# Optimization experiments

Measured on AMD Instinct MI355X. Metric: run time of the kernel, lower is better.

## Reference

```python
import jax, jax.numpy as jnp
import numpy as np

H_RENDER = 640   # hard-coded render resolution in the torch forward
W_RENDER = 640
OUT_H = 128      # self.height
OUT_W = 128      # self.width
NUM_VERTS = 778  # MANO hand mesh
NUM_FACES = 1538
BATCH = 4
BG_DEPTH = 1e10  # z-buffer background, clamped to 100 afterwards


def setup_inputs() -> dict:
    key = jax.random.key(0)
    k1, k2, k3 = jax.random.split(key, 3)
    # screen-space x,y in [0, 640), positive depth z
    xy = jax.random.uniform(k1, (BATCH, NUM_VERTS, 2), minval=0.0, maxval=640.0)
    z = jax.random.uniform(k2, (BATCH, NUM_VERTS, 1), minval=0.3, maxval=1.5)
    vertices = jnp.concatenate([xy, z], axis=-1).astype(jnp.float32)
    faces = jax.random.randint(k3, (NUM_FACES, 3), 0, NUM_VERTS)
    # right_hand=True: swap face columns 0 and 1 (winding flip), as in __init__
    faces = faces[:, jnp.array([1, 0, 2])].astype(jnp.int64)
    return {"vertices": vertices, "faces": faces}


def _edge(ax, ay, bx, by, px, py):
    # signed area of (a, b, p); standard rasterizer edge function
    return (bx - ax) * (py - ay) - (by - ay) * (px - ax)


def _rasterize(face_vertices):
    # face_vertices: [B, F, 3(vertex), 3(x,y,z)] -> z-buffer depth map [B, H, W]
    B = face_vertices.shape[0]
    ys, xs = jnp.meshgrid(
        jnp.arange(H_RENDER, dtype=jnp.float32) + 0.5,
        jnp.arange(W_RENDER, dtype=jnp.float32) + 0.5,
        indexing='ij',
    )  # pixel centers, [H, W]

    def step(zbuf, tri):
        # tri: [B, 3, 3] -> per-vertex coords broadcast to [B, 1, 1]
        x = tri[:, :, 0][:, :, None, None]
        y = tri[:, :, 1][:, :, None, None]
        z = tri[:, :, 2][:, :, None, None]
        x0, x1, x2 = x[:, 0], x[:, 1], x[:, 2]
        y0, y1, y2 = y[:, 0], y[:, 1], y[:, 2]
        z0, z1, z2 = z[:, 0], z[:, 1], z[:, 2]
        e0 = _edge(x1, y1, x2, y2, xs, ys)  # weight of v0
        e1 = _edge(x2, y2, x0, y0, xs, ys)  # weight of v1
        e2 = _edge(x0, y0, x1, y1, xs, ys)  # weight of v2
        area = _edge(x0, y0, x1, y1, x2, y2)  # [B,1,1]
        s = jnp.sign(area)
        valid = jnp.abs(area) > 1e-12
        inside = (e0 * s >= 0) & (e1 * s >= 0) & (e2 * s >= 0) & valid
        safe_area = jnp.where(valid, area, 1.0)
        zpix = (e0 * z0 + e1 * z1 + e2 * z2) / safe_area  # barycentric depth
        cand = jnp.where(inside, zpix, jnp.float32(BG_DEPTH))
        return jnp.minimum(zbuf, cand), None

    zbuf0 = jnp.full((B, H_RENDER, W_RENDER), BG_DEPTH, dtype=jnp.float32)
    zbuf, _ = jax.lax.scan(step, zbuf0, jnp.swapaxes(face_vertices, 0, 1))
    return zbuf


def reference(vertices, faces):
    B = vertices.shape[0]
    F = faces.shape[0]
    # vertex gather: vertices[:, faces.view(-1), 0:3].view(B, F, 3, 3)
    fv = vertices[:, faces.reshape(-1), 0:3].reshape(B, F, 3, 3)
    dm = _rasterize(fv)
    dm = jnp.minimum(dm, 100.0)  # torch.clamp(max=100.0)
    # bilinear resize, align_corners=False (half-pixel), no antialias, like F.interpolate
    resized = jax.image.resize(dm[:, None], (B, 1, OUT_H, OUT_W), method='linear', antialias=False)
    return resized[:, 0]
```

## Files before the change

kernel.cpp:

```cpp
#include <hip/hip_runtime.h>


#pragma clang fp contract(off)

#define H_OUT 128
#define W_OUT 128
#define NV 778
#define NF 1538
#define NB 4
#define NCHUNK 25
#define NFP (NCHUNK * 64)
#define BG100 0x42C80000u


__global__ __launch_bounds__(256) void prep_kernel(
    const float* __restrict__ verts,
    const int* __restrict__ faces,
    float* __restrict__ bbox,
    float* __restrict__ data,
    unsigned int* __restrict__ outu)
{
    int t = blockIdx.x * 256 + threadIdx.x;
    outu[t] = BG100;
    if (t >= NB * NFP) return;
    int b = t / NFP;
    int f = t - b * NFP;
    float* bb = bbox + (size_t)t * 4;
    if (f >= NF) {
        bb[0] = 1e30f; bb[1] = -1e30f; bb[2] = 1e30f; bb[3] = -1e30f;
        return;
    }
    int i0 = faces[f * 3 + 0];
    int i1 = faces[f * 3 + 1];
    int i2 = faces[f * 3 + 2];
    const float* vb = verts + (size_t)b * NV * 3;
    float x0 = vb[i0 * 3 + 0], y0 = vb[i0 * 3 + 1], z0 = vb[i0 * 3 + 2];
    float x1 = vb[i1 * 3 + 0], y1 = vb[i1 * 3 + 1], z1 = vb[i1 * 3 + 2];
    float x2 = vb[i2 * 3 + 0], y2 = vb[i2 * 3 + 1], z2 = vb[i2 * 3 + 2];

    float dx12 = x2 - x1, dy12 = y2 - y1;
    float dx02 = x0 - x2, dy02 = y0 - y2;
    float dx01 = x1 - x0, dy01 = y1 - y0;
    float y20 = y2 - y0, x20 = x2 - x0;
    float area = dx01 * y20 - dy01 * x20;

    float s = 0.0f;
    if (fabsf(area) > 1e-12f) s = (area > 0.0f) ? 1.0f : -1.0f;

    float xmin = fminf(fminf(x0, x1), x2), xmax = fmaxf(fmaxf(x0, x1), x2);
    float ymin = fminf(fminf(y0, y1), y2), ymax = fmaxf(fmaxf(y0, y1), y2);
    if (s == 0.0f) { xmin = 1e30f; xmax = -1e30f; }

    bb[0] = xmin; bb[1] = xmax; bb[2] = ymin; bb[3] = ymax;

    float* o = data + (size_t)t * 16;
    o[0] = s * dx12; o[1] = s * dy12;
    o[2] = s * dx02; o[3] = s * dy02;
    o[4] = s * dx01; o[5] = s * dy01;
    o[6] = x0;  o[7] = y0;  o[8] = x1;  o[9] = y1;  o[10] = x2; o[11] = y2;
    o[12] = z0; o[13] = z1; o[14] = z2; o[15] = s * area;
}

__global__ __launch_bounds__(128) void raster_kernel(
    const float* __restrict__ bbox,
    const float* __restrict__ data,
    unsigned int* __restrict__ outu)
{
    int blk = blockIdx.x;
    int tile  = blk & 127;
    int b     = (blk >> 7) & 3;
    int chunk = blk >> 9;
    int tid = threadIdx.x;
    int lane = tid & 63;
    int w = __builtin_amdgcn_readfirstlane(tid >> 6);

    int tx = tile & 7, ty = tile >> 3;
    int i = ty * 8 + w * 4 + (lane >> 4);
    int j = tx * 16 + (lane & 15);
    float px = 5.0f * (float)j + 2.5f;
    float py = 5.0f * (float)i + 2.5f;

    float px_lo = 80.0f * (float)tx + 2.5f, px_hi = px_lo + 75.0f;
    float py_lo = 40.0f * (float)ty + 20.0f * (float)w + 2.5f;
    float py_hi = py_lo + 15.0f;

    int gbase = b * NFP + chunk * 64;
    float4 bb = *(const float4*)&bbox[(size_t)(gbase + lane) * 4];
    bool ov = !(bb.x > px_hi || bb.y < px_lo || bb.z > py_hi || bb.w < py_lo);
    unsigned long long mask = __ballot(ov);

    float nb = 1e10f, ab = 1.0f;
    while (mask) {
        int f0 = __builtin_ctzll(mask); mask &= mask - 1;
        int f1 = mask ? __builtin_ctzll(mask) : f0;
        mask &= mask - 1;

        int u0 = __builtin_amdgcn_readfirstlane(f0);
        int u1 = __builtin_amdgcn_readfirstlane(f1);
        const float4* p0 = (const float4*)(data + (size_t)(gbase + u0) * 16);
        const float4* p1 = (const float4*)(data + (size_t)(gbase + u1) * 16);
        float4 A0 = p0[0], B0 = p0[1], C0 = p0[2], D0 = p0[3];
        float4 A1 = p1[0], B1 = p1[1], C1 = p1[2], D1 = p1[3];

        float e0 = A0.x * (py - C0.y) - A0.y * (px - C0.x);
        float e1 = A0.z * (py - C0.w) - A0.w * (px - C0.z);
        float e2 = B0.x * (py - B0.w) - B0.y * (px - B0.z);
        bool in0 = (e0 >= 0.0f) & (e1 >= 0.0f) & (e2 >= 0.0f);
        float n0 = ((e0 * D0.x) + (e1 * D0.y)) + (e2 * D0.z);
        bool t0 = in0 & (n0 * ab < nb * D0.w);
        nb = t0 ? n0 : nb;  ab = t0 ? D0.w : ab;

        float g0 = A1.x * (py - C1.y) - A1.y * (px - C1.x);
        float g1 = A1.z * (py - C1.w) - A1.w * (px - C1.z);
        float g2 = B1.x * (py - B1.w) - B1.y * (px - B1.z);
        bool in1 = (g0 >= 0.0f) & (g1 >= 0.0f) & (g2 >= 0.0f);
        float n1 = ((g0 * D1.x) + (g1 * D1.y)) + (g2 * D1.z);
        bool t1 = in1 & (n1 * ab < nb * D1.w);
        nb = t1 ? n1 : nb;  ab = t1 ? D1.w : ab;
    }

    float z = nb / ab;
    z += 0.0f;
    if (z < 1e9f)
        atomicMin(&outu[(size_t)b * (H_OUT * W_OUT) + i * W_OUT + j],
                  __float_as_uint(fminf(z, 100.0f)));
}

extern "C" void kernel_launch(void* const* d_in, const int* in_sizes, int n_in,
                              void* d_out, int out_size, void* d_ws, size_t ws_size,
                              hipStream_t stream) {
    const float* verts = (const float*)d_in[0];
    const int*   faces = (const int*)d_in[1];
    float* out = (float*)d_out;
    float* bbox = (float*)d_ws;
    float* data = bbox + (size_t)NB * NFP * 4;

    prep_kernel<<<256, 256, 0, stream>>>(verts, faces, bbox, data,
                                         (unsigned int*)out);
    raster_kernel<<<NCHUNK * NB * 128, 128, 0, stream>>>(
        bbox, data, (unsigned int*)out);
}
```

Before: 93.00 us.

## Process four pixel rows per lane with one wave per 16x16 tile

```diff
diff --git a/kernel.cpp b/kernel.cpp
--- a/kernel.cpp
+++ b/kernel.cpp
@@ -61,35 +61,38 @@
     o[12] = z0; o[13] = z1; o[14] = z2; o[15] = s * area;
 }
 
-__global__ __launch_bounds__(128) void raster_kernel(
+__global__ __launch_bounds__(64) void raster_kernel(
     const float* __restrict__ bbox,
     const float* __restrict__ data,
     unsigned int* __restrict__ outu)
 {
     int blk = blockIdx.x;
-    int tile  = blk & 127;
-    int b     = (blk >> 7) & 3;
-    int chunk = blk >> 9;
-    int tid = threadIdx.x;
-    int lane = tid & 63;
-    int w = __builtin_amdgcn_readfirstlane(tid >> 6);
+    int tile  = blk & 63;
+    int b     = (blk >> 6) & 3;
+    int chunk = blk >> 8;
+    int lane = threadIdx.x;
 
     int tx = tile & 7, ty = tile >> 3;
-    int i = ty * 8 + w * 4 + (lane >> 4);
-    int j = tx * 16 + (lane & 15);
-    float px = 5.0f * (float)j + 2.5f;
-    float py = 5.0f * (float)i + 2.5f;
+    int col = lane & 15;
+    int rg  = lane >> 4;
+    int j = tx * 16 + col;
+    int i0r = ty * 16 + rg;
+    float px  = 5.0f * (float)j + 2.5f;
+    float py0 = 5.0f * (float)i0r + 2.5f;
 
     float px_lo = 80.0f * (float)tx + 2.5f, px_hi = px_lo + 75.0f;
-    float py_lo = 40.0f * (float)ty + 20.0f * (float)w + 2.5f;
-    float py_hi = py_lo + 15.0f;
+    float py_lo = 80.0f * (float)ty + 2.5f, py_hi = py_lo + 75.0f;
 
     int gbase = b * NFP + chunk * 64;
     float4 bb = *(const float4*)&bbox[(size_t)(gbase + lane) * 4];
     bool ov = !(bb.x > px_hi || bb.y < px_lo || bb.z > py_hi || bb.w < py_lo);
     unsigned long long mask = __ballot(ov);
 
-    float nb = 1e10f, ab = 1.0f;
+    float nb0 = 1e10f, ab0 = 1.0f;
+    float nb1 = 1e10f, ab1 = 1.0f;
+    float nb2 = 1e10f, ab2 = 1.0f;
+    float nb3 = 1e10f, ab3 = 1.0f;
+
     while (mask) {
         int f0 = __builtin_ctzll(mask); mask &= mask - 1;
         int f1 = mask ? __builtin_ctzll(mask) : f0;
@@ -102,28 +105,43 @@
         float4 A0 = p0[0], B0 = p0[1], C0 = p0[2], D0 = p0[3];
         float4 A1 = p1[0], B1 = p1[1], C1 = p1[2], D1 = p1[3];
 
-        float e0 = A0.x * (py - C0.y) - A0.y * (px - C0.x);
-        float e1 = A0.z * (py - C0.w) - A0.w * (px - C0.z);
-        float e2 = B0.x * (py - B0.w) - B0.y * (px - B0.z);
-        bool in0 = (e0 >= 0.0f) & (e1 >= 0.0f) & (e2 >= 0.0f);
-        float n0 = ((e0 * D0.x) + (e1 * D0.y)) + (e2 * D0.z);
-        bool t0 = in0 & (n0 * ab < nb * D0.w);
-        nb = t0 ? n0 : nb;  ab = t0 ? D0.w : ab;
+        #pragma unroll
+        for (int k = 0; k < 4; ++k) {
+            float py = py0 + 20.0f * (float)k;
+            float* nbp = (k == 0) ? &nb0 : (k == 1) ? &nb1 : (k == 2) ? &nb2 : &nb3;
+            float* abp = (k == 0) ? &ab0 : (k == 1) ? &ab1 : (k == 2) ? &ab2 : &ab3;
+            float nb = *nbp, ab = *abp;
 
-        float g0 = A1.x * (py - C1.y) - A1.y * (px - C1.x);
-        float g1 = A1.z * (py - C1.w) - A1.w * (px - C1.z);
-        float g2 = B1.x * (py - B1.w) - B1.y * (px - B1.z);
-        bool in1 = (g0 >= 0.0f) & (g1 >= 0.0f) & (g2 >= 0.0f);
-        float n1 = ((g0 * D1.x) + (g1 * D1.y)) + (g2 * D1.z);
-        bool t1 = in1 & (n1 * ab < nb * D1.w);
-        nb = t1 ? n1 : nb;  ab = t1 ? D1.w : ab;
+            float e0 = A0.x * (py - C0.y) - A0.y * (px - C0.x);
+            float e1 = A0.z * (py - C0.w) - A0.w * (px - C0.z);
+            float e2 = B0.x * (py - B0.w) - B0.y * (px - B0.z);
+            bool in0 = (e0 >= 0.0f) & (e1 >= 0.0f) & (e2 >= 0.0f);
+            float n0 = ((e0 * D0.x) + (e1 * D0.y)) + (e2 * D0.z);
+            bool t0 = in0 & (n0 * ab < nb * D0.w);
+            nb = t0 ? n0 : nb;  ab = t0 ? D0.w : ab;
+
+            float h0 = A1.x * (py - C1.y) - A1.y * (px - C1.x);
+            float h1 = A1.z * (py - C1.w) - A1.w * (px - C1.z);
+            float h2 = B1.x * (py - B1.w) - B1.y * (px - B1.z);
+            bool in1 = (h0 >= 0.0f) & (h1 >= 0.0f) & (h2 >= 0.0f);
+            float n1 = ((h0 * D1.x) + (h1 * D1.y)) + (h2 * D1.z);
+            bool t1 = in1 & (n1 * ab < nb * D1.w);
+            nb = t1 ? n1 : nb;  ab = t1 ? D1.w : ab;
+
+            *nbp = nb; *abp = ab;
+        }
     }
 
-    float z = nb / ab;
-    z += 0.0f;
-    if (z < 1e9f)
-        atomicMin(&outu[(size_t)b * (H_OUT * W_OUT) + i * W_OUT + j],
-                  __float_as_uint(fminf(z, 100.0f)));
+    unsigned int* slot0 = &outu[(size_t)b * (H_OUT * W_OUT) + i0r * W_OUT + j];
+    #pragma unroll
+    for (int k = 0; k < 4; ++k) {
+        float nb = (k == 0) ? nb0 : (k == 1) ? nb1 : (k == 2) ? nb2 : nb3;
+        float ab = (k == 0) ? ab0 : (k == 1) ? ab1 : (k == 2) ? ab2 : ab3;
+        float z = nb / ab;
+        z += 0.0f;
+        if (z < 1e9f)
+            atomicMin(slot0 + k * 4 * W_OUT, __float_as_uint(fminf(z, 100.0f)));
+    }
 }
 
 extern "C" void kernel_launch(void* const* d_in, const int* in_sizes, int n_in,
@@ -137,6 +155,6 @@
 
     prep_kernel<<<256, 256, 0, stream>>>(verts, faces, bbox, data,
                                          (unsigned int*)out);
-    raster_kernel<<<NCHUNK * NB * 128, 128, 0, stream>>>(
+    raster_kernel<<<NCHUNK * NB * 64, 64, 0, stream>>>(
         bbox, data, (unsigned int*)out);
 }
```

Result: slower. 97.02 us (+4.3%).
